# Optimization experiments

Measured on AMD Instinct MI355X. Metric: run time of the kernel, lower is better.

## Reference

```python
import jax, jax.numpy as jnp
import numpy as np

B, S, D, H, DH = 2, 2048, 1024, 16, 64
ATTN_SCALE = float(np.sqrt(DH))  # use_attn_scale=True -> sqrt(d_head)
IGNORE = -100000.0


def setup_inputs() -> dict:
    key = jax.random.key(0)
    ks = jax.random.split(key, 8)
    init = 0.02
    return {
        "residual": jax.random.normal(ks[0], (B, S, D), dtype=jnp.float32),
        "x": jax.random.normal(ks[1], (B, S, D), dtype=jnp.float32),
        "W_Q": jax.random.normal(ks[2], (H, D, DH), dtype=jnp.float32) * init,
        "W_K": jax.random.normal(ks[3], (H, D, DH), dtype=jnp.float32) * init,
        "W_V": jax.random.normal(ks[4], (H, D, DH), dtype=jnp.float32) * init,
        "W_O": jax.random.normal(ks[5], (H, DH, D), dtype=jnp.float32) * init,
        "b_Q": jnp.zeros((H, DH), dtype=jnp.float32),
        "b_K": jnp.zeros((H, DH), dtype=jnp.float32),
        "b_V": jnp.zeros((H, DH), dtype=jnp.float32),
        "b_O": jnp.zeros((D,), dtype=jnp.float32),
    }


def reference(residual, x, W_Q, W_K, W_V, W_O, b_Q, b_K, b_V, b_O):
    # QKV projections: [b,s,d] x [h,d,e] -> [b,s,h,e]
    q = jnp.einsum("bsd,hde->bshe", x, W_Q) + b_Q
    k = jnp.einsum("bsd,hde->bshe", x, W_K) + b_K
    v = jnp.einsum("bsd,hde->bshe", x, W_V) + b_V
    # Scores: [b,h,q,k]
    attn_scores = jnp.einsum("bqhe,bkhe->bhqk", q, k) / ATTN_SCALE
    causal = jnp.tril(jnp.ones((S, S), dtype=bool))
    attn_scores = jnp.where(causal, attn_scores, IGNORE)
    pattern = jax.nn.softmax(attn_scores, axis=-1)
    # Weighted values: [b,q,h,e]
    z = jnp.einsum("bkhe,bhqk->bqhe", v, pattern)
    out = jnp.einsum("bqhe,hed->bqd", z, W_O) + b_O
    return (residual, out)
```

## Files before the change

### kernel.cpp

```cpp
#include <hip/hip_runtime.h>
#include <hip/hip_bf16.h>

#define BB 2
#define SS 2048
#define DD 1024
#define HH 16
#define DHD 64

typedef __attribute__((ext_vector_type(8))) short short8;
typedef __attribute__((ext_vector_type(4))) float floatx4;

static __device__ __forceinline__ unsigned short f2bf(float f) {
    union { __hip_bfloat16 h; unsigned short u; } cv;
    cv.h = __float2bfloat16(f);
    return cv.u;
}

typedef __attribute__((address_space(1))) const unsigned int* gas_t;
typedef __attribute__((address_space(3))) unsigned int* las_t;
static __device__ __forceinline__ void g2l16(const void* g, void* l) {
    __builtin_amdgcn_global_load_lds((gas_t)g, (las_t)l, 16, 0, 0);
}

#define SW(row, c8) ((c8) ^ ((row) & 7))

__global__ __launch_bounds__(256) void prep(const float4* __restrict__ residual4,
        float4* __restrict__ out4,
        const float* __restrict__ x, unsigned short* __restrict__ xb,
        const float* __restrict__ WQ, const float* __restrict__ WK,
        const float* __restrict__ WV, unsigned short* __restrict__ Wt,
        const float* __restrict__ WO, unsigned short* __restrict__ WtO) {
    __shared__ float tile[64][65];
    const int bid = blockIdx.x;
    const int t = threadIdx.x;

    if (bid < 1024) {
        size_t base = (size_t)bid * 1024 + t;
#pragma unroll
        for (int j = 0; j < 4; j++) out4[base + j * 256] = residual4[base + j * 256];
    } else if (bid < 3072) {
        size_t i = ((size_t)(bid - 1024) * 256 + t) * 8;
        const float* src = x + i;
        short8 o;
#pragma unroll
        for (int j = 0; j < 8; j++) o[j] = (short)f2bf(src[j]);
        *(short8*)(xb + i) = o;
    } else if (bid < 3840) {
        int u = bid - 3072;
        const int d0 = (u & 15) * 64;
        const int h  = (u >> 4) & 15;
        const int which = u >> 8;
        const float* W = (which == 0) ? WQ : (which == 1) ? WK : WV;
        const float* src = W + (size_t)h * DD * DHD;
#pragma unroll
        for (int i = 0; i < 16; i++) {
            int idx = i * 256 + t;
            int r = idx >> 6, c = idx & 63;
            tile[r][c] = src[(size_t)(d0 + r) * DHD + c];
        }
        __syncthreads();
        unsigned short* dst = Wt + ((size_t)which * 1024 + h * 64) * DD;
#pragma unroll
        for (int i = 0; i < 16; i++) {
            int idx = i * 256 + t;
            int e = idx >> 6, d = idx & 63;
            dst[(size_t)e * DD + d0 + d] = f2bf(tile[d][e]);
        }
    } else {
        int u = bid - 3840;
        const int k0 = (u & 15) * 64;
        const int n0 = (u >> 4) * 64;
#pragma unroll
        for (int i = 0; i < 16; i++) {
            int idx = i * 256 + t;
            int r = idx >> 6, c = idx & 63;
            tile[r][c] = WO[(size_t)(k0 + r) * DD + n0 + c];
        }
        __syncthreads();
#pragma unroll
        for (int i = 0; i < 16; i++) {
            int idx = i * 256 + t;
            int n = idx >> 6, kk = idx & 63;
            WtO[(size_t)(n0 + n) * DD + k0 + kk] = f2bf(tile[kk][n]);
        }
    }
}

__global__ __launch_bounds__(256) void qkv_mfma(const unsigned short* __restrict__ xb,
        const unsigned short* __restrict__ Wt,
        const float* __restrict__ bQ, const float* __restrict__ bK,
        const float* __restrict__ bV,
        unsigned short* __restrict__ oq, unsigned short* __restrict__ ok,
        unsigned short* __restrict__ ov) {
    __shared__ unsigned short smem[128 * 132];
    unsigned short* As = smem;
    unsigned short* Bs = smem + 128 * 64;

    const int m0 = blockIdx.x * 128;
    const int y  = blockIdx.y;
    const int which = y >> 3;
    const int h0 = (y & 7) * 2;
    const float* bias = (which == 0) ? bQ : (which == 1) ? bK : bV;
    unsigned short* ob = (which == 0) ? oq : (which == 1) ? ok : ov;
    const float scale = (which == 0) ? 0.125f : 1.0f;
    const unsigned short* Wb = Wt + (size_t)y * 128 * DD;

    const int t = threadIdx.x;
    const int lane = t & 63, w = t >> 6;
    const int l15 = lane & 15, quad = lane >> 4;

    floatx4 acc[2][8];
#pragma unroll
    for (int mt = 0; mt < 2; mt++)
#pragma unroll
        for (int nt = 0; nt < 8; nt++) acc[mt][nt] = floatx4{0.f, 0.f, 0.f, 0.f};

    for (int k0 = 0; k0 < DD; k0 += 64) {
#pragma unroll
        for (int i = 0; i < 4; i++) {
            int c = i * 256 + t;
            int row = c >> 3, c8 = c & 7;
            g2l16(xb + (size_t)(m0 + row) * DD + k0 + SW(row, c8) * 8, As + c * 8);
        }
#pragma unroll
        for (int i = 0; i < 4; i++) {
            int c = i * 256 + t;
            int row = c >> 3, c8 = c & 7;
            g2l16(Wb + (size_t)row * DD + k0 + SW(row, c8) * 8, Bs + c * 8);
        }
        __syncthreads();
#pragma unroll
        for (int ks = 0; ks < 2; ks++) {
            short8 af[2], bf[8];
#pragma unroll
            for (int mt = 0; mt < 2; mt++)
                af[mt] = *(const short8*)(As + (w * 32 + mt * 16 + l15) * 64 +
                                          SW(l15, ks * 4 + quad) * 8);
#pragma unroll
            for (int nt = 0; nt < 8; nt++)
                bf[nt] = *(const short8*)(Bs + (nt * 16 + l15) * 64 +
                                          SW(l15, ks * 4 + quad) * 8);
#pragma unroll
            for (int mt = 0; mt < 2; mt++)
#pragma unroll
                for (int nt = 0; nt < 8; nt++)
                    acc[mt][nt] = __builtin_amdgcn_mfma_f32_16x16x32_bf16(
                        af[mt], bf[nt], acc[mt][nt], 0, 0, 0);
        }
        __syncthreads();
    }

    if (which == 2) {
        unsigned short* T = smem;
#pragma unroll
        for (int mt = 0; mt < 2; mt++)
#pragma unroll
            for (int r = 0; r < 4; r++) {
                int mloc = w * 32 + mt * 16 + quad * 4 + r;
#pragma unroll
                for (int nt = 0; nt < 8; nt++) {
                    int n = nt * 16 + l15;
                    int h = h0 + (n >> 6), e = n & 63;
                    T[n * 132 + mloc] = f2bf(acc[mt][nt][r] + bias[h * DHD + e]);
                }
            }
        __syncthreads();
        const int b = m0 >> 11;
        const int s_base = m0 & (SS - 1);
#pragma unroll
        for (int i = 0; i < 8; i++) {
            int u = i * 256 + t;
            int row = u >> 4, c8 = u & 15;
            int h = h0 + (row >> 6), e = row & 63;
            *(short8*)(ov + (((size_t)b * HH + h) * DHD + e) * SS + s_base + c8 * 8) =
                *(const short8*)(T + row * 132 + c8 * 8);
        }
    } else {
#pragma unroll
        for (int mt = 0; mt < 2; mt++) {
#pragma unroll
            for (int r = 0; r < 4; r++) {
                int m = m0 + w * 32 + mt * 16 + quad * 4 + r;
                int b = m >> 11, s = m & (SS - 1);
#pragma unroll
                for (int nt = 0; nt < 8; nt++) {
                    int h = h0 + (nt >> 2);
                    int e = (nt & 3) * 16 + l15;
                    float v = (acc[mt][nt][r] + bias[h * DHD + e]) * scale;
                    ob[(((size_t)b * HH + h) * SS + s) * DHD + e] = f2bf(v);
                }
            }
        }
    }
}

#define KSTRIDE 72
#define VSTRIDE 136
__global__ __launch_bounds__(512) void attn(const unsigned short* __restrict__ q,
        const unsigned short* __restrict__ k, const unsigned short* __restrict__ vt,
        unsigned short* __restrict__ z) {
    __shared__ unsigned short Ks[128 * KSTRIDE];
    __shared__ unsigned short Vt[64 * VSTRIDE];
    __shared__ unsigned short Ps[8 * 16 * VSTRIDE];

    const int i0 = blockIdx.x;
    int bh, qt;
    if (i0 < 256) { bh = i0 & 31;         qt = 15 - (i0 >> 5); }
    else          { bh = (i0 - 256) & 31; qt = (i0 - 256) >> 5; }
    const int b  = bh >> 4, h = bh & (HH - 1);
    const int q0 = qt * 128;

    const int t = threadIdx.x;
    const int lane = t & 63;
    const int w = t >> 6;
    const int l15 = lane & 15;
    const int quad = lane >> 4;

    const unsigned short* qb  = q  + (size_t)bh * SS * DHD;
    const unsigned short* kb  = k  + (size_t)bh * SS * DHD;
    const unsigned short* vtb = vt + (size_t)bh * DHD * SS;

    short8 a_frag[2];
#pragma unroll
    for (int c = 0; c < 2; c++)
        a_frag[c] = *(const short8*)(qb +
            (size_t)(q0 + w * 16 + l15) * DHD + c * 32 + quad * 8);

    float lsum[4];
    floatx4 o_acc[4];
#pragma unroll
    for (int r = 0; r < 4; r++) lsum[r] = 0.f;
#pragma unroll
    for (int nt = 0; nt < 4; nt++) o_acc[nt] = floatx4{0.f, 0.f, 0.f, 0.f};

    unsigned short* Psw = Ps + w * 16 * VSTRIDE;
    const int fmin = q0 + w * 16;
    const int wave_max_row = fmin + 15;
    const int nkt = qt + 1;

    for (int kt = 0; kt < nkt; kt++) {
        __syncthreads();
#pragma unroll
        for (int i = 0; i < 2; i++) {
            int u = i * 512 + t;
            int row = u >> 3, c8 = u & 7;
            *(short8*)(Ks + row * KSTRIDE + c8 * 8) =
                *(const short8*)(kb + (size_t)(kt * 128 + row) * DHD + c8 * 8);
        }
#pragma unroll
        for (int i = 0; i < 2; i++) {
            int u = i * 512 + t;
            int e = u >> 4, c8 = u & 15;
            *(short8*)(Vt + e * VSTRIDE + c8 * 8) =
                *(const short8*)(vtb + (size_t)e * SS + kt * 128 + c8 * 8);
        }
        __syncthreads();

        floatx4 sacc[8];
#pragma unroll
        for (int nt = 0; nt < 8; nt++) {
            const int kb0 = kt * 128 + nt * 16;
            if (kb0 > wave_max_row) {
                sacc[nt] = floatx4{-1e30f, -1e30f, -1e30f, -1e30f};
            } else {
                short8 bf0 = *(const short8*)(Ks + (nt * 16 + l15) * KSTRIDE +
                                              quad * 8);
                short8 bf1 = *(const short8*)(Ks + (nt * 16 + l15) * KSTRIDE +
                                              32 + quad * 8);
                floatx4 acc = {0.f, 0.f, 0.f, 0.f};
                acc = __builtin_amdgcn_mfma_f32_16x16x32_bf16(a_frag[0], bf0, acc,
                                                              0, 0, 0);
                acc = __builtin_amdgcn_mfma_f32_16x16x32_bf16(a_frag[1], bf1, acc,
                                                              0, 0, 0);
                if (kb0 + 15 > fmin) {
#pragma unroll
                    for (int r = 0; r < 4; r++)
                        if (kb0 + l15 > fmin + quad * 4 + r) acc[r] = -1e30f;
                }
                sacc[nt] = acc;
            }
        }

#pragma unroll
        for (int r = 0; r < 4; r++) {
            float ps = 0.f;
#pragma unroll
            for (int nt = 0; nt < 8; nt++) {
                float pv = __expf(sacc[nt][r]);
                ps += pv;
                Psw[(quad * 4 + r) * VSTRIDE + nt * 16 + l15] = f2bf(pv);
            }
            lsum[r] += ps;
        }

        short8 pa[4];
#pragma unroll
        for (int ks = 0; ks < 4; ks++)
            pa[ks] = *(const short8*)(Psw + l15 * VSTRIDE + ks * 32 + quad * 8);
#pragma unroll
        for (int nt = 0; nt < 4; nt++) {
#pragma unroll
            for (int ks = 0; ks < 4; ks++) {
                short8 bf = *(const short8*)(Vt + (nt * 16 + l15) * VSTRIDE +
                                             ks * 32 + quad * 8);
                o_acc[nt] = __builtin_amdgcn_mfma_f32_16x16x32_bf16(
                    pa[ks], bf, o_acc[nt], 0, 0, 0);
            }
        }
    }

#pragma unroll
    for (int r = 0; r < 4; r++) {
        float s = lsum[r];
#pragma unroll
        for (int off = 1; off < 16; off <<= 1) s += __shfl_xor(s, off);
        float inv = 1.f / s;
        int qrow = q0 + w * 16 + quad * 4 + r;
        unsigned short* zr = z + ((size_t)b * SS + qrow) * (HH * DHD) + h * DHD;
#pragma unroll
        for (int nt = 0; nt < 4; nt++)
            zr[nt * 16 + l15] = f2bf(o_acc[nt][r] * inv);
    }
}

__global__ __launch_bounds__(256) void out_mfma(const unsigned short* __restrict__ zb,
        const unsigned short* __restrict__ WtO, const float* __restrict__ bo,
        float* __restrict__ out) {
    __shared__ unsigned short As[64 * 64];
    __shared__ unsigned short Bs[128 * 64];

    const int m0 = blockIdx.x * 64;
    const int n0 = blockIdx.y * 128;
    const int t = threadIdx.x;
    const int lane = t & 63, w = t >> 6;
    const int l15 = lane & 15, quad = lane >> 4;

    floatx4 acc[8];
#pragma unroll
    for (int nt = 0; nt < 8; nt++) acc[nt] = floatx4{0.f, 0.f, 0.f, 0.f};

    for (int k0 = 0; k0 < DD; k0 += 64) {
#pragma unroll
        for (int i = 0; i < 2; i++) {
            int c = i * 256 + t;
            int row = c >> 3, c8 = c & 7;
            g2l16(zb + (size_t)(m0 + row) * DD + k0 + SW(row, c8) * 8, As + c * 8);
        }
#pragma unroll
        for (int i = 0; i < 4; i++) {
            int c = i * 256 + t;
            int row = c >> 3, c8 = c & 7;
            g2l16(WtO + (size_t)(n0 + row) * DD + k0 + SW(row, c8) * 8, Bs + c * 8);
        }
        __syncthreads();
#pragma unroll
        for (int ks = 0; ks < 2; ks++) {
            short8 af = *(const short8*)(As + (w * 16 + l15) * 64 +
                                         SW(l15, ks * 4 + quad) * 8);
#pragma unroll
            for (int nt = 0; nt < 8; nt++) {
                short8 bf = *(const short8*)(Bs + (nt * 16 + l15) * 64 +
                                             SW(l15, ks * 4 + quad) * 8);
                acc[nt] = __builtin_amdgcn_mfma_f32_16x16x32_bf16(
                    af, bf, acc[nt], 0, 0, 0);
            }
        }
        __syncthreads();
    }
#pragma unroll
    for (int r = 0; r < 4; r++) {
        int m = m0 + w * 16 + quad * 4 + r;
#pragma unroll
        for (int nt = 0; nt < 8; nt++) {
            int n = n0 + nt * 16 + l15;
            out[(size_t)m * DD + n] = acc[nt][r] + bo[n];
        }
    }
}

extern "C" void kernel_launch(void* const* d_in, const int* in_sizes, int n_in,
                              void* d_out, int out_size, void* d_ws, size_t ws_size,
                              hipStream_t stream) {
    const float* residual = (const float*)d_in[0];
    const float* x   = (const float*)d_in[1];
    const float* W_Q = (const float*)d_in[2];
    const float* W_K = (const float*)d_in[3];
    const float* W_V = (const float*)d_in[4];
    const float* W_O = (const float*)d_in[5];
    const float* b_Q = (const float*)d_in[6];
    const float* b_K = (const float*)d_in[7];
    const float* b_V = (const float*)d_in[8];
    const float* b_O = (const float*)d_in[9];
    float* out = (float*)d_out;

    const size_t NE = (size_t)BB * SS * HH * DHD;
    unsigned short* xb  = (unsigned short*)d_ws;
    unsigned short* Wt  = xb + (size_t)4096 * 1024;
    unsigned short* WtO = Wt + (size_t)3072 * 1024;
    unsigned short* qb  = WtO + (size_t)1024 * 1024;
    unsigned short* kb  = qb + NE;
    unsigned short* vb  = kb + NE;
    unsigned short* zb  = vb + NE;

    prep<<<4096, 256, 0, stream>>>((const float4*)residual, (float4*)out,
                                   x, xb, W_Q, W_K, W_V, Wt, W_O, WtO);

    qkv_mfma<<<dim3(32, 24), 256, 0, stream>>>(xb, Wt, b_Q, b_K, b_V, qb, kb, vb);

    attn<<<512, 512, 0, stream>>>(qb, kb, vb, zb);

    out_mfma<<<dim3(64, 8), 256, 0, stream>>>(
        zb, WtO, b_O, out + (size_t)BB * SS * DD);
}
```

Baseline: 212.4 us.

## Rewrite attention with 32x32 MFMA, register-resident P, and double-buffered async K/V loads

The attention kernel now uses 32x32x16 bf16 MFMAs with 4 waves of 32 query rows each, in place of 16x16 tiles over 8 waves. Scores are computed transposed (K as A, Q as B), so the exp'd probabilities are packed to bf16 and rearranged with permlane32 swaps directly into B operands for the PV MFMA. This removes the round trip of P through LDS. K/V tiles of 64 are double-buffered and prefetched with global_load_lds into XOR-swizzled LDS, cutting a barrier and overlapping loads with compute. The trade-offs are higher register pressure and a smaller block, and it relies on gfx950-specific instructions.

```diff
diff --git a/kernel.cpp b/kernel.cpp
--- a/kernel.cpp
+++ b/kernel.cpp
@@ -9,6 +9,8 @@
 
 typedef __attribute__((ext_vector_type(8))) short short8;
 typedef __attribute__((ext_vector_type(4))) float floatx4;
+typedef __attribute__((ext_vector_type(16))) float floatx16;
+typedef __attribute__((ext_vector_type(4))) unsigned short ushortx4;
 
 static __device__ __forceinline__ unsigned short f2bf(float f) {
     union { __hip_bfloat16 h; unsigned short u; } cv;
@@ -23,6 +25,15 @@
 }
 
 #define SW(row, c8) ((c8) ^ ((row) & 7))
+
+static __device__ __forceinline__ unsigned cvt_pk_bf16(float lo, float hi) {
+    unsigned r;
+    asm("v_cvt_pk_bf16_f32 %0, %1, %2" : "=v"(r) : "v"(lo), "v"(hi));
+    return r;
+}
+static __device__ __forceinline__ void pl32_swap(unsigned &a, unsigned &b) {
+    asm("v_permlane32_swap_b32 %0, %1" : "+v"(a), "+v"(b));
+}
 
 __global__ __launch_bounds__(256) void prep(const float4* __restrict__ residual4,
         float4* __restrict__ out4,
@@ -194,14 +205,12 @@
     }
 }
 
-#define KSTRIDE 72
-#define VSTRIDE 136
-__global__ __launch_bounds__(512) void attn(const unsigned short* __restrict__ q,
+#define KVB 64
+__global__ __launch_bounds__(256) void attn(const unsigned short* __restrict__ q,
         const unsigned short* __restrict__ k, const unsigned short* __restrict__ vt,
         unsigned short* __restrict__ z) {
-    __shared__ unsigned short Ks[128 * KSTRIDE];
-    __shared__ unsigned short Vt[64 * VSTRIDE];
-    __shared__ unsigned short Ps[8 * 16 * VSTRIDE];
+    __shared__ unsigned short Ks[2][KVB * 64];
+    __shared__ unsigned short Vs[2][KVB * 64];
 
     const int i0 = blockIdx.x;
     int bh, qt;
@@ -213,114 +222,126 @@
     const int t = threadIdx.x;
     const int lane = t & 63;
     const int w = t >> 6;
-    const int l15 = lane & 15;
-    const int quad = lane >> 4;
+    const int l31 = lane & 31;
+    const int hi = lane >> 5;
 
     const unsigned short* qb  = q  + (size_t)bh * SS * DHD;
     const unsigned short* kb  = k  + (size_t)bh * SS * DHD;
     const unsigned short* vtb = vt + (size_t)bh * DHD * SS;
 
-    short8 a_frag[2];
-#pragma unroll
-    for (int c = 0; c < 2; c++)
-        a_frag[c] = *(const short8*)(qb +
-            (size_t)(q0 + w * 16 + l15) * DHD + c * 32 + quad * 8);
-
-    float lsum[4];
-    floatx4 o_acc[4];
-#pragma unroll
-    for (int r = 0; r < 4; r++) lsum[r] = 0.f;
-#pragma unroll
-    for (int nt = 0; nt < 4; nt++) o_acc[nt] = floatx4{0.f, 0.f, 0.f, 0.f};
-
-    unsigned short* Psw = Ps + w * 16 * VSTRIDE;
-    const int fmin = q0 + w * 16;
-    const int wave_max_row = fmin + 15;
-    const int nkt = qt + 1;
+    const int qrow = q0 + w * 32 + l31;
+    short8 qf[4];
+#pragma unroll
+    for (int c = 0; c < 4; c++)
+        qf[c] = *(const short8*)(qb + (size_t)qrow * DHD + c * 16 + hi * 8);
+
+    floatx16 o_acc[2];
+#pragma unroll
+    for (int eh = 0; eh < 2; eh++)
+#pragma unroll
+        for (int i = 0; i < 16; i++) o_acc[eh][i] = 0.f;
+    float lsum = 0.f;
+
+    const int nkt = 2 * qt + 2;
+    const int wqmax = q0 + w * 32 + 31;
+
+#pragma unroll
+    for (int i = 0; i < 2; i++) {
+        int u = i * 256 + t, r = u >> 3, c8 = u & 7;
+        g2l16(kb + (size_t)r * DHD + SW(r, c8) * 8, &Ks[0][u * 8]);
+    }
+#pragma unroll
+    for (int i = 0; i < 2; i++) {
+        int u = i * 256 + t, r = u >> 3, c8 = u & 7;
+        g2l16(vtb + (size_t)r * SS + SW(r, c8) * 8, &Vs[0][u * 8]);
+    }
 
     for (int kt = 0; kt < nkt; kt++) {
-        __syncthreads();
-#pragma unroll
-        for (int i = 0; i < 2; i++) {
-            int u = i * 512 + t;
-            int row = u >> 3, c8 = u & 7;
-            *(short8*)(Ks + row * KSTRIDE + c8 * 8) =
-                *(const short8*)(kb + (size_t)(kt * 128 + row) * DHD + c8 * 8);
-        }
-#pragma unroll
-        for (int i = 0; i < 2; i++) {
-            int u = i * 512 + t;
-            int e = u >> 4, c8 = u & 15;
-            *(short8*)(Vt + e * VSTRIDE + c8 * 8) =
-                *(const short8*)(vtb + (size_t)e * SS + kt * 128 + c8 * 8);
-        }
-        __syncthreads();
-
-        floatx4 sacc[8];
-#pragma unroll
-        for (int nt = 0; nt < 8; nt++) {
-            const int kb0 = kt * 128 + nt * 16;
-            if (kb0 > wave_max_row) {
-                sacc[nt] = floatx4{-1e30f, -1e30f, -1e30f, -1e30f};
-            } else {
-                short8 bf0 = *(const short8*)(Ks + (nt * 16 + l15) * KSTRIDE +
-                                              quad * 8);
-                short8 bf1 = *(const short8*)(Ks + (nt * 16 + l15) * KSTRIDE +
-                                              32 + quad * 8);
-                floatx4 acc = {0.f, 0.f, 0.f, 0.f};
-                acc = __builtin_amdgcn_mfma_f32_16x16x32_bf16(a_frag[0], bf0, acc,
-                                                              0, 0, 0);
-                acc = __builtin_amdgcn_mfma_f32_16x16x32_bf16(a_frag[1], bf1, acc,
-                                                              0, 0, 0);
-                if (kb0 + 15 > fmin) {
-#pragma unroll
-                    for (int r = 0; r < 4; r++)
-                        if (kb0 + l15 > fmin + quad * 4 + r) acc[r] = -1e30f;
-                }
-                sacc[nt] = acc;
-            }
-        }
-
-#pragma unroll
-        for (int r = 0; r < 4; r++) {
-            float ps = 0.f;
-#pragma unroll
-            for (int nt = 0; nt < 8; nt++) {
-                float pv = __expf(sacc[nt][r]);
-                ps += pv;
-                Psw[(quad * 4 + r) * VSTRIDE + nt * 16 + l15] = f2bf(pv);
-            }
-            lsum[r] += ps;
-        }
-
-        short8 pa[4];
-#pragma unroll
-        for (int ks = 0; ks < 4; ks++)
-            pa[ks] = *(const short8*)(Psw + l15 * VSTRIDE + ks * 32 + quad * 8);
-#pragma unroll
-        for (int nt = 0; nt < 4; nt++) {
-#pragma unroll
-            for (int ks = 0; ks < 4; ks++) {
-                short8 bf = *(const short8*)(Vt + (nt * 16 + l15) * VSTRIDE +
-                                             ks * 32 + quad * 8);
-                o_acc[nt] = __builtin_amdgcn_mfma_f32_16x16x32_bf16(
-                    pa[ks], bf, o_acc[nt], 0, 0, 0);
-            }
-        }
-    }
-
-#pragma unroll
-    for (int r = 0; r < 4; r++) {
-        float s = lsum[r];
-#pragma unroll
-        for (int off = 1; off < 16; off <<= 1) s += __shfl_xor(s, off);
-        float inv = 1.f / s;
-        int qrow = q0 + w * 16 + quad * 4 + r;
-        unsigned short* zr = z + ((size_t)b * SS + qrow) * (HH * DHD) + h * DHD;
-#pragma unroll
-        for (int nt = 0; nt < 4; nt++)
-            zr[nt * 16 + l15] = f2bf(o_acc[nt][r] * inv);
-    }
+        const int cur = kt & 1;
+        __syncthreads();
+        if (kt + 1 < nkt) {
+            const int nxt = cur ^ 1;
+            const int kbase = (kt + 1) * KVB;
+#pragma unroll
+            for (int i = 0; i < 2; i++) {
+                int u = i * 256 + t, r = u >> 3, c8 = u & 7;
+                g2l16(kb + (size_t)(kbase + r) * DHD + SW(r, c8) * 8, &Ks[nxt][u * 8]);
+            }
+#pragma unroll
+            for (int i = 0; i < 2; i++) {
+                int u = i * 256 + t, r = u >> 3, c8 = u & 7;
+                g2l16(vtb + (size_t)r * SS + kbase + SW(r, c8) * 8, &Vs[nxt][u * 8]);
+            }
+        }
+
+        short8 pb[4];
+        bool alive[2];
+#pragma unroll
+        for (int st = 0; st < 2; st++) {
+            const int kvb = kt * KVB + st * 32;
+            alive[st] = (kvb <= wqmax);
+            if (!alive[st]) continue;
+
+            floatx16 sacc;
+#pragma unroll
+            for (int i = 0; i < 16; i++) sacc[i] = 0.f;
+#pragma unroll
+            for (int c = 0; c < 4; c++) {
+                const int row = st * 32 + l31;
+                short8 af = *(const short8*)(
+                    &Ks[cur][row * 64 + SW(row, 2 * c + hi) * 8]);
+                sacc = __builtin_amdgcn_mfma_f32_32x32x16_bf16(af, qf[c], sacc,
+                                                               0, 0, 0);
+            }
+
+            unsigned wv[8];
+#pragma unroll
+            for (int r2 = 0; r2 < 8; r2++) {
+                const int ra = 2 * r2, rb = 2 * r2 + 1;
+                const int kva = kvb + (ra & 3) + 8 * (ra >> 2) + 4 * hi;
+                const int kvbr = kvb + (rb & 3) + 8 * (rb >> 2) + 4 * hi;
+                float p0 = (kva  <= qrow) ? __expf(sacc[ra]) : 0.f;
+                float p1 = (kvbr <= qrow) ? __expf(sacc[rb]) : 0.f;
+                lsum += p0 + p1;
+                wv[r2] = cvt_pk_bf16(p0, p1);
+            }
+            pl32_swap(wv[0], wv[2]);
+            pl32_swap(wv[1], wv[3]);
+            pl32_swap(wv[4], wv[6]);
+            pl32_swap(wv[5], wv[7]);
+            union { unsigned u[4]; short8 s; } u0, u1;
+            u0.u[0] = wv[0]; u0.u[1] = wv[1]; u0.u[2] = wv[2]; u0.u[3] = wv[3];
+            u1.u[0] = wv[4]; u1.u[1] = wv[5]; u1.u[2] = wv[6]; u1.u[3] = wv[7];
+            pb[2 * st]     = u0.s;
+            pb[2 * st + 1] = u1.s;
+        }
+
+#pragma unroll
+        for (int ch = 0; ch < 4; ch++) {
+            if (!alive[ch >> 1]) continue;
+#pragma unroll
+            for (int eh = 0; eh < 2; eh++) {
+                const int e = eh * 32 + l31;
+                short8 vf = *(const short8*)(
+                    &Vs[cur][e * 64 + SW(e, 2 * ch + hi) * 8]);
+                o_acc[eh] = __builtin_amdgcn_mfma_f32_32x32x16_bf16(
+                    vf, pb[ch], o_acc[eh], 0, 0, 0);
+            }
+        }
+    }
+
+    lsum += __shfl_xor(lsum, 32);
+    const float inv = 1.f / lsum;
+    unsigned short* zr = z + ((size_t)b * SS + qrow) * (HH * DHD) + h * DHD;
+#pragma unroll
+    for (int eh = 0; eh < 2; eh++)
+#pragma unroll
+        for (int g = 0; g < 4; g++) {
+            ushortx4 o;
+#pragma unroll
+            for (int m = 0; m < 4; m++) o[m] = f2bf(o_acc[eh][g * 4 + m] * inv);
+            *(ushortx4*)(zr + eh * 32 + g * 8 + 4 * hi) = o;
+        }
 }
 
 __global__ __launch_bounds__(256) void out_mfma(const unsigned short* __restrict__ zb,
@@ -407,7 +428,7 @@
 
     qkv_mfma<<<dim3(32, 24), 256, 0, stream>>>(xb, Wt, b_Q, b_K, b_V, qb, kb, vb);
 
-    attn<<<512, 512, 0, stream>>>(qb, kb, vb, zb);
+    attn<<<512, 256, 0, stream>>>(qb, kb, vb, zb);
 
     out_mfma<<<dim3(64, 8), 256, 0, stream>>>(
         zb, WtO, b_O, out + (size_t)BB * SS * DD);
```

New measurement: 233.2 us. 9.8% more time.
